# Kernel optimization log

Measured on AMD Instinct MI355X. Metric: run time of the kernel, lower is better.

Reference implementation:

```python
import jax, jax.numpy as jnp
import numpy as np

B, N, E, S, A, P, T = 512, 65536, 131072, 256, 512, 2, 64


def setup_inputs() -> dict:
    key = jax.random.key(0)
    ks = jax.random.split(key, 40)
    f32 = jnp.float32

    def g(i, shape, s=0.05):
        return jax.random.normal(ks[i], shape, f32) * s

    inp = {
        'nodes': jax.random.normal(ks[0], (N, S), f32),
        'edge_features': jax.random.normal(ks[1], (E, S), f32),
        'edge_source': jax.random.randint(ks[2], (E,), 0, N),
        'edge_dest': jax.random.randint(ks[3], (E,), 0, N),
        'node_owner': jax.random.randint(ks[4], (N,), 0, B),
        'running': jnp.ones((B,), bool),
        'ref_types': jax.random.randint(ks[5], (B,), 0, T),
        # decision aggregator (transform + sigmoid gate)
        'dec_t_W': g(6, (A, S)), 'dec_t_b': g(7, (A,)),
        'dec_g_W': g(8, (A, S)), 'dec_g_b': jnp.ones((A,), f32),
        # init aggregator
        'init_t_W': g(9, (A, S)), 'init_t_b': g(10, (A,)),
        'init_g_W': g(11, (A, S)), 'init_g_b': jnp.ones((A,), f32),
        # node type decision head + embedding
        'ntd_W': g(12, (T + 1, A)), 'ntd_b': g(13, (T + 1,)),
        'nte': g(14, (T, S), 1.0),
        # f_init
        'f1_W': g(15, (S, S)), 'f1_b': g(16, (S,)),
        'f2_W': g(17, (S, A)),
        # propagator params, stacked over P steps (message_size = 2S)
        'mn_W': g(18, (P, 2 * S, S)),
        'mf_W': g(19, (P, 2 * S, S)),
        'ml2_W': g(20, (P, 2 * S, 2 * S)), 'ml2_b': g(21, (P, 2 * S)),
        'gru_Wih': g(22, (P, 3 * S, 2 * S)), 'gru_Whh': g(23, (P, 3 * S, S)),
        'gru_bih': jnp.zeros((P, 3 * S), f32),
        'gru_bhh': jnp.concatenate(
            [jnp.ones((P, S), f32), jnp.zeros((P, 2 * S), f32)], axis=-1),
    }
    return inp


def _aggregate(nodes, fmask, tW, tb, gW, gb):
    # Aggregator.forward: sigmoid gate * linear transform, pooled per graph
    # via dense 0/1 owner-mask matmul (dropout=0 -> identity).
    gates = jax.nn.sigmoid(nodes @ gW.T + gb)
    data = nodes @ tW.T + tb
    return fmask @ (data * gates)  # [B, A]


def reference(nodes, edge_features, edge_source, edge_dest, node_owner,
              running, ref_types,
              dec_t_W, dec_t_b, dec_g_W, dec_g_b,
              init_t_W, init_t_b, init_g_W, init_g_b,
              ntd_W, ntd_b, nte, f1_W, f1_b, f2_W,
              mn_W, mf_W, ml2_W, ml2_b, gru_Wih, gru_Whh, gru_bih, gru_bhh):
    f32 = nodes.dtype
    fmask = (node_owner[None, :] == jnp.arange(B)[:, None]).astype(f32)  # [B,N]
    # Propagator._node_update_mask: owner_masks[running].sum(0) > 0
    upd = (fmask * running[:, None].astype(f32)).sum(0) > 0  # [N]

    for p in range(P):
        ef = edge_features @ mf_W[p].T                 # [E, 2S]
        nf = nodes @ mn_W[p].T                         # [N, 2S]
        msgs = nf[edge_source] + nf[edge_dest] + ef
        msgs = jnp.tanh(msgs) @ ml2_W[p].T + ml2_b[p]  # message_layer_2
        inputs = jnp.zeros((N, 2 * S), f32)
        inputs = inputs.at[edge_dest].add(msgs).at[edge_source].add(msgs)
        # torch GRUCell (gate order r, z, n)
        gi = inputs @ gru_Wih[p].T + gru_bih[p]
        gh = nodes @ gru_Whh[p].T + gru_bhh[p]
        ir, iz, inn = jnp.split(gi, 3, axis=-1)
        hr, hz, hn = jnp.split(gh, 3, axis=-1)
        r = jax.nn.sigmoid(ir + hr)
        z = jax.nn.sigmoid(iz + hz)
        n = jnp.tanh(inn + r * hn)
        new_nodes = (1.0 - z) * n + z * nodes
        nodes = jnp.where(upd[:, None], new_nodes, nodes)

    # node-type decision
    agg = _aggregate(nodes, fmask, dec_t_W, dec_t_b, dec_g_W, dec_g_b)
    logits = agg @ ntd_W.T + ntd_b                      # [B, T+1]

    # training path: remap_pad (no pad chars present) -> ref + 1
    sel = ref_types + 1                                  # in [1, T]
    logp = jax.nn.log_softmax(logits, axis=-1)
    per_ex = -logp[jnp.arange(B), sel]
    loss = jnp.where(running, per_ex, 0.0).mean()

    # new node features for running graphs
    emb = nte[sel - 1]                                   # [B, S]
    init_feats = _aggregate(nodes, fmask, init_t_W, init_t_b,
                            init_g_W, init_g_b)
    new_features = emb @ f1_W.T + f1_b + init_feats @ f2_W.T  # [B, S]
    return logits, new_features, loss
```

## Files before the change

### kernel.cpp

```cpp
#include <hip/hip_runtime.h>
#include <hip/hip_bf16.h>
#include <math.h>

#define BG 512
#define NN 65536
#define EE 131072
#define SD 256
#define AD 512
#define PP 2
#define TD 64

typedef __attribute__((ext_vector_type(8))) short sx8;
typedef __attribute__((ext_vector_type(4))) short sx4;
typedef __attribute__((ext_vector_type(4))) float fx4;

__device__ __forceinline__ float bs2f(short s) {
    union { unsigned u; float f; } x; x.u = ((unsigned)(unsigned short)s) << 16; return x.f;
}
__device__ __forceinline__ short f2bs(float f) {
    union { float f; unsigned u; } x; x.f = f;
    unsigned r = x.u + 0x7fffu + ((x.u >> 16) & 1u);
    return (short)(r >> 16);
}
__device__ __forceinline__ float fast_tanh(float x) {
    float xc = fminf(fmaxf(x, -15.f), 15.f);
    float e = __expf(2.f * xc);
    return __fdividef(e - 1.f, e + 1.f);
}
__device__ __forceinline__ float fast_sigm(float x) {
    float xc = fminf(fmaxf(x, -30.f), 30.f);
    float e = __expf(-xc);
    return __fdividef(1.f, 1.f + e);
}
__device__ __forceinline__ bool run_flag(const void* runv, int idx) {
    const unsigned char* r8 = (const unsigned char*)runv;
    const int* r32 = (const int*)runv;
    return (r8[idx] != 0) || (r32[idx] != 0);
}

__device__ __forceinline__ void gload16(const short* g, short* l) {
    __builtin_amdgcn_global_load_lds(
        (const __attribute__((address_space(1))) void*)g,
        (__attribute__((address_space(3))) void*)l, 16, 0, 0);
}

template<int EPI>
__launch_bounds__(256, 4)
__global__ void gemm_bt(const short* __restrict__ Abp, const short* __restrict__ Wp,
                        const float* __restrict__ bias, const float* __restrict__ bias2,
                        short* __restrict__ Cout, short* __restrict__ Fout,
                        short* __restrict__ FoutB,
                        const float* __restrict__ biasB, const float* __restrict__ biasB2,
                        const short* __restrict__ nfp,
                        const int* __restrict__ esrc, const int* __restrict__ edst,
                        int K, int NC, int NT, int nsplit)
{
    __shared__ __align__(16) short sA[2 * 4096];
    __shared__ __align__(16) short sB[2 * 4096];
    const int t = threadIdx.x;
    const int lane = t & 63;
    const int w = t >> 6;

    const int nwg = gridDim.x;
    const int q = nwg >> 3;
    const int wg = (blockIdx.x & 7) * q + (blockIdx.x >> 3);
    const int mt = wg / NT;
    const int nt = wg - mt * NT;
    const int m0 = mt * 128;
    const int n0 = nt * 128;

    const int wm = (w >> 1) * 64;
    const int wn = (w & 1) * 64;
    const int lr = lane & 15;
    const int lg = lane >> 4;

    fx4 acc[4][4];
#pragma unroll
    for (int i = 0; i < 4; i++)
#pragma unroll
        for (int j = 0; j < 4; j++) { fx4 z = {0.f, 0.f, 0.f, 0.f}; acc[i][j] = z; }

    const int r = t >> 2;
    const int cblk = (t & 3) ^ ((r >> 1) & 3);
    const short* gA = Abp + (size_t)(m0 + r) * K + cblk * 8;
    const short* gB = Wp + (size_t)(n0 + r) * K + cblk * 8;
    const size_t rowskip = (size_t)64 * K;

    auto STAGE = [&](int b, int kk) {
        gload16(gA + kk,           sA + b * 4096 + w * 512);
        gload16(gA + kk + rowskip, sA + b * 4096 + 2048 + w * 512);
        gload16(gB + kk,           sB + b * 4096 + w * 512);
        gload16(gB + kk + rowskip, sB + b * 4096 + 2048 + w * 512);
    };

    STAGE(0, 0);

    int es[4], ed[4];
    if (EPI == 2) {
#pragma unroll
        for (int mi = 0; mi < 4; mi++) {
            const int m = m0 + wm + mi * 16 + lr;
            es[mi] = esrc[m]; ed[mi] = edst[m];
        }
    }

    __syncthreads();
    int buf = 0;
    const int xa = (lr >> 1) & 3;
    for (int kk = 0; kk < K; kk += 32) {
        if (kk + 32 < K) STAGE(buf ^ 1, kk + 32);
        const short* cA = sA + buf * 4096;
        const short* cB = sB + buf * 4096;
        sx8 af[4], bfr[4];
#pragma unroll
        for (int mi = 0; mi < 4; mi++)
            af[mi] = *(const sx8*)(cA + (wm + mi * 16 + lr) * 32 + (lg ^ xa) * 8);
#pragma unroll
        for (int ni = 0; ni < 4; ni++)
            bfr[ni] = *(const sx8*)(cB + (wn + ni * 16 + lr) * 32 + (lg ^ xa) * 8);
#pragma unroll
        for (int mi = 0; mi < 4; mi++)
#pragma unroll
            for (int ni = 0; ni < 4; ni++) {
                if (EPI == 4)
                    acc[mi][ni] = __builtin_amdgcn_mfma_f32_16x16x32_bf16(
                        af[mi], bfr[ni], acc[mi][ni], 0, 0, 0);
                else
                    acc[mi][ni] = __builtin_amdgcn_mfma_f32_16x16x32_bf16(
                        bfr[ni], af[mi], acc[mi][ni], 0, 0, 0);
            }
        __syncthreads();
        buf ^= 1;
    }

    if (EPI == 4) {
        const bool useB = (n0 >= nsplit);
        short* fo = useB ? FoutB : Fout;
        const float* tb = useB ? biasB : bias;
        const float* gb = useB ? biasB2 : bias2;
        const int ln0 = useB ? (n0 - nsplit) : n0;
#pragma unroll
        for (int mi = 0; mi < 4; mi++) {
#pragma unroll
            for (int rg = 0; rg < 4; rg++) {
                const int m = m0 + wm + mi * 16 + lg * 4 + rg;
#pragma unroll
                for (int ni = 0; ni < 4; ni += 2) {
                    const int rc = (((ln0 + wn + ni * 16) >> 5) << 4) + lr;
                    float dv = acc[mi][ni][rg] + tb[rc];
                    float gv = fast_sigm(acc[mi][ni + 1][rg] + gb[rc]);
                    fo[(size_t)m * 512 + rc] = f2bs(dv * gv);
                }
            }
        }
    } else {
#pragma unroll
        for (int mi = 0; mi < 4; mi++) {
            const int m = m0 + wm + mi * 16 + lr;
            if (EPI == 2) {
                const short* ps = nfp + (size_t)es[mi] * NC + n0;
                const short* pd = nfp + (size_t)ed[mi] * NC + n0;
                short* co = Cout + (size_t)m * NC + n0;
#pragma unroll
                for (int ni = 0; ni < 4; ni++) {
                    const int nc = wn + ni * 16 + lg * 4;
                    sx4 a4 = *(const sx4*)(ps + nc);
                    sx4 b4 = *(const sx4*)(pd + nc);
                    sx4 o;
#pragma unroll
                    for (int rg = 0; rg < 4; rg++)
                        o[rg] = f2bs(fast_tanh(acc[mi][ni][rg]
                                               + bs2f(a4[rg]) + bs2f(b4[rg])));
                    *(sx4*)(co + nc) = o;
                }
            } else {
                short* co = Cout + (size_t)m * NC + n0;
#pragma unroll
                for (int ni = 0; ni < 4; ni++) {
                    const int nc = wn + ni * 16 + lg * 4;
                    fx4 vb = {0.f, 0.f, 0.f, 0.f};
                    if (bias) vb = *(const fx4*)(bias + n0 + nc);
                    sx4 o;
#pragma unroll
                    for (int rg = 0; rg < 4; rg++)
                        o[rg] = f2bs(acc[mi][ni][rg] + vb[rg]);
                    *(sx4*)(co + nc) = o;
                }
            }
        }
    }
}

__global__ void k_castw(const float* __restrict__ in, short* __restrict__ out)
{
    size_t i = ((size_t)blockIdx.x * 256 + threadIdx.x) * 4;
    fx4 v = *(const fx4*)(in + i);
    sx4 o;
#pragma unroll
    for (int u = 0; u < 4; u++) o[u] = f2bs(v[u]);
    *(sx4*)(out + i) = o;
}

__global__ void k_cast_pair(const float* __restrict__ tW, const float* __restrict__ gW,
                            short* __restrict__ out)
{
    size_t i = ((size_t)blockIdx.x * 256 + threadIdx.x) * 4;
    const int r2 = (int)(i >> 8);
    const int c = (int)(i & 255);
    const int src = ((r2 >> 5) << 4) | (r2 & 15);
    const float* W = ((r2 >> 4) & 1) ? gW : tW;
    fx4 v = *(const fx4*)(W + (size_t)src * 256 + c);
    sx4 o;
#pragma unroll
    for (int u = 0; u < 4; u++) o[u] = f2bs(v[u]);
    *(sx4*)(out + i) = o;
}

__global__ void k_count2(const int* __restrict__ a, const int* __restrict__ b,
                         int* __restrict__ deg, int n)
{
    int i = blockIdx.x * 256 + threadIdx.x;
    if (i < n) { atomicAdd(&deg[a[i]], 1); atomicAdd(&deg[b[i]], 1); }
}
__global__ void k_count1(const int* __restrict__ a, int* __restrict__ deg, int n)
{
    int i = blockIdx.x * 256 + threadIdx.x;
    if (i < n) atomicAdd(&deg[a[i]], 1);
}
__global__ void k_scan(const int* __restrict__ deg, int* __restrict__ offs, int n)
{
    __shared__ int part[256];
    const int t = threadIdx.x;
    const int chunk = n >> 8;
    const int base = t * chunk;
    int s = 0;
    for (int i = 0; i < chunk; i++) s += deg[base + i];
    part[t] = s;
    __syncthreads();
    for (int off = 1; off < 256; off <<= 1) {
        int v = (t >= off) ? part[t - off] : 0;
        __syncthreads();
        part[t] += v;
        __syncthreads();
    }
    int run = (t > 0) ? part[t - 1] : 0;
    for (int i = 0; i < chunk; i++) {
        offs[base + i] = run;
        run += deg[base + i];
    }
    if (t == 255) offs[n] = part[255];
}
__global__ void k_fill2(const int* __restrict__ a, const int* __restrict__ b,
                        const int* __restrict__ offs, int* __restrict__ cur,
                        int* __restrict__ elist, int n)
{
    int i = blockIdx.x * 256 + threadIdx.x;
    if (i < n) {
        int p = atomicAdd(&cur[a[i]], 1); elist[offs[a[i]] + p] = i;
        int q = atomicAdd(&cur[b[i]], 1); elist[offs[b[i]] + q] = i;
    }
}
__global__ void k_fill1(const int* __restrict__ own, const int* __restrict__ offs,
                        int* __restrict__ cur, int* __restrict__ nlist, int n)
{
    int i = blockIdx.x * 256 + threadIdx.x;
    if (i < n) {
        int p = atomicAdd(&cur[own[i]], 1); nlist[offs[own[i]] + p] = i;
    }
}

__global__ void k_edge_gather(const short* __restrict__ msgs, const int* __restrict__ offs,
                              const int* __restrict__ elist, short* __restrict__ inp)
{
    const int node = blockIdx.x * 4 + (threadIdx.x >> 6);
    const int c = (threadIdx.x & 63) * 8;
    const int s0 = offs[node], s1 = offs[node + 1];
    float acc[8] = {0.f, 0.f, 0.f, 0.f, 0.f, 0.f, 0.f, 0.f};
    for (int s = s0; s < s1; s++) {
        const int e = elist[s];
        sx8 v = *(const sx8*)(msgs + (size_t)e * 512 + c);
#pragma unroll
        for (int u = 0; u < 8; u++) acc[u] += bs2f(v[u]);
    }
    sx8 o;
#pragma unroll
    for (int u = 0; u < 8; u++) o[u] = f2bs(acc[u]);
    *(sx8*)(inp + (size_t)node * 512 + c) = o;
}

__global__ void k_owner_reduce(const short* __restrict__ gp, const int* __restrict__ offsB,
                               const int* __restrict__ nlist, float* __restrict__ agg)
{
    const int b = blockIdx.x, t = threadIdx.x;
    const int s0 = offsB[b], s1 = offsB[b + 1];
    float a0 = 0.f, a1 = 0.f;
    for (int s = s0; s < s1; s++) {
        const int n = nlist[s];
        const short* pp = gp + (size_t)n * 512 + t * 2;
        a0 += bs2f(pp[0]); a1 += bs2f(pp[1]);
    }
    agg[(size_t)b * 512 + t * 2] = a0;
    agg[(size_t)b * 512 + t * 2 + 1] = a1;
}

__global__ void k_gru(const short* __restrict__ gi, const short* __restrict__ gh,
                      short* __restrict__ nodes,
                      const int* __restrict__ owner, const void* __restrict__ runv)
{
    const int n = blockIdx.x * 4 + (threadIdx.x >> 6);
    const int t = threadIdx.x & 63;
    const bool run = run_flag(runv, owner[n]);
    const size_t gb = (size_t)n * 768 + t * 4;
    sx4 vir = *(const sx4*)(gi + gb);
    sx4 viz = *(const sx4*)(gi + gb + 256);
    sx4 vin = *(const sx4*)(gi + gb + 512);
    sx4 whr = *(const sx4*)(gh + gb);
    sx4 whz = *(const sx4*)(gh + gb + 256);
    sx4 whn = *(const sx4*)(gh + gb + 512);
    const size_t nbase = (size_t)n * 256 + t * 4;
    sx4 old4 = *(const sx4*)(nodes + nbase);
    sx4 outb;
#pragma unroll
    for (int u = 0; u < 4; u++) {
        float old = bs2f(old4[u]);
        float rr = fast_sigm(bs2f(vir[u]) + bs2f(whr[u]));
        float zz = fast_sigm(bs2f(viz[u]) + bs2f(whz[u]));
        float nn = fast_tanh(bs2f(vin[u]) + rr * bs2f(whn[u]));
        float nv = (1.f - zz) * nn + zz * old;
        outb[u] = run ? f2bs(nv) : old4[u];
    }
    *(sx4*)(nodes + nbase) = outb;
}

__global__ void k_logits(const float* __restrict__ agg, const float* __restrict__ Wt,
                         const float* __restrict__ bt, float* __restrict__ logitsF,
                         float* __restrict__ outL)
{
    __shared__ float row[512];
    const int b = blockIdx.x, t = threadIdx.x;
    for (int k = t; k < 512; k += 128) row[k] = agg[(size_t)b * 512 + k];
    __syncthreads();
    if (t < TD + 1) {
        float acc = bt[t];
        const float* wr = Wt + (size_t)t * 512;
        for (int k = 0; k < 512; k++) acc += row[k] * wr[k];
        logitsF[b * (TD + 1) + t] = acc;
        outL[b * (TD + 1) + t] = acc;
    }
}

__global__ void k_loss(const float* __restrict__ logitsF, const int* __restrict__ reft,
                       const void* __restrict__ runv, float* __restrict__ outLoss)
{
    __shared__ float red[512];
    const int b = threadIdx.x;
    const float* lr = logitsF + b * (TD + 1);
    float mx = lr[0];
    for (int k = 1; k < TD + 1; k++) mx = fmaxf(mx, lr[k]);
    float se = 0.f;
    for (int k = 0; k < TD + 1; k++) se += expf(lr[k] - mx);
    const int sel = reft[b] + 1;
    float pe = logf(se) + mx - lr[sel];
    red[b] = run_flag(runv, b) ? pe : 0.f;
    __syncthreads();
    for (int s = 256; s > 0; s >>= 1) {
        if (b < s) red[b] += red[b + s];
        __syncthreads();
    }
    if (b == 0) outLoss[0] = red[0] / (float)BG;
}

__global__ void k_newfeat(const float* __restrict__ aggi, const float* __restrict__ nte,
                          const int* __restrict__ reft, const float* __restrict__ f1W,
                          const float* __restrict__ f1b, const float* __restrict__ f2W,
                          float* __restrict__ outNF)
{
    __shared__ float emb[256];
    __shared__ float ag[512];
    const int b = blockIdx.x, t = threadIdx.x;
    const int rt = reft[b];
    emb[t] = nte[(size_t)rt * 256 + t];
    ag[t] = aggi[(size_t)b * 512 + t];
    ag[t + 256] = aggi[(size_t)b * 512 + 256 + t];
    __syncthreads();
    float acc = f1b[t];
    const float* w1 = f1W + (size_t)t * 256;
    for (int k = 0; k < 256; k++) acc += emb[k] * w1[k];
    const float* w2 = f2W + (size_t)t * 512;
    for (int a = 0; a < 512; a++) acc += ag[a] * w2[a];
    outNF[(size_t)b * 256 + t] = acc;
}

extern "C" void kernel_launch(void* const* d_in, const int* in_sizes, int n_in,
                              void* d_out, int out_size, void* d_ws, size_t ws_size,
                              hipStream_t stream)
{
    (void)in_sizes; (void)n_in; (void)out_size;
    const float* in_nodes = (const float*)d_in[0];
    const float* in_ef    = (const float*)d_in[1];
    const int*   e_src    = (const int*)d_in[2];
    const int*   e_dst    = (const int*)d_in[3];
    const int*   owner    = (const int*)d_in[4];
    const void*  running  = d_in[5];
    const int*   reft     = (const int*)d_in[6];
    const float* dec_tW = (const float*)d_in[7];
    const float* dec_tb = (const float*)d_in[8];
    const float* dec_gW = (const float*)d_in[9];
    const float* dec_gb = (const float*)d_in[10];
    const float* init_tW = (const float*)d_in[11];
    const float* init_tb = (const float*)d_in[12];
    const float* init_gW = (const float*)d_in[13];
    const float* init_gb = (const float*)d_in[14];
    const float* ntdW = (const float*)d_in[15];
    const float* ntdb = (const float*)d_in[16];
    const float* nte  = (const float*)d_in[17];
    const float* f1W  = (const float*)d_in[18];
    const float* f1b  = (const float*)d_in[19];
    const float* f2W  = (const float*)d_in[20];
    const float* mnW  = (const float*)d_in[21];
    const float* mfW  = (const float*)d_in[22];
    const float* ml2W = (const float*)d_in[23];
    const float* ml2b = (const float*)d_in[24];
    const float* Wih  = (const float*)d_in[25];
    const float* Whh  = (const float*)d_in[26];
    const float* bih  = (const float*)d_in[27];
    const float* bhh  = (const float*)d_in[28];

    float* outL    = (float*)d_out;
    float* outNF   = outL + BG * (TD + 1);
    float* outLoss = outNF + BG * SD;

    size_t off = 0;
    auto take = [&](size_t bytes) -> void* {
        void* p = (char*)d_ws + off;
        off += (bytes + 255) & ~(size_t)255;
        return p;
    };
    short* nodes_bf  = (short*)take((size_t)NN * SD * 2);
    short* ef_bf     = (short*)take((size_t)EE * SD * 2);
    short* bufC      = (short*)take((size_t)NN * 512 * 2);
    short* bufD      = (short*)take((size_t)EE * 512 * 2);
    short* bufM      = (short*)take((size_t)EE * 512 * 2);
    short* bufI      = (short*)take((size_t)NN * 512 * 2);
    float* aggD      = (float*)take((size_t)BG * AD * 4);
    float* aggI      = (float*)take((size_t)BG * AD * 4);
    float* logitsF   = (float*)take((size_t)BG * (TD + 1) * 4);
    short* mnWb  = (short*)take((size_t)PP * 512 * 256 * 2);
    short* mfWb  = (short*)take((size_t)PP * 512 * 256 * 2);
    short* ml2Wb = (short*)take((size_t)PP * 512 * 512 * 2);
    short* WihB  = (short*)take((size_t)PP * 768 * 512 * 2);
    short* WhhB  = (short*)take((size_t)PP * 768 * 256 * 2);
    short* W4agg = (short*)take((size_t)2048 * 256 * 2);
    int* deg_e = (int*)take((size_t)NN * 4);
    int* offs_e = (int*)take((size_t)(NN + 1) * 4);
    int* cur_e = (int*)take((size_t)NN * 4);
    int* elist = (int*)take((size_t)2 * EE * 4);
    int* degB = (int*)take((size_t)BG * 4);
    int* offsB = (int*)take((size_t)(BG + 1) * 4);
    int* curB = (int*)take((size_t)BG * 4);
    int* nlist = (int*)take((size_t)NN * 4);
    if (off > ws_size) return;

    short* gi = bufD;
    short* gh = bufM;
    short* gpD = bufM;
    short* gpI = bufD;

    k_castw<<<NN * SD / 1024, 256, 0, stream>>>(in_nodes, nodes_bf);
    k_castw<<<EE * SD / 1024, 256, 0, stream>>>(in_ef, ef_bf);
    k_castw<<<PP * 512 * 256 / 1024, 256, 0, stream>>>(mnW, mnWb);
    k_castw<<<PP * 512 * 256 / 1024, 256, 0, stream>>>(mfW, mfWb);
    k_castw<<<PP * 512 * 512 / 1024, 256, 0, stream>>>(ml2W, ml2Wb);
    k_castw<<<PP * 768 * 512 / 1024, 256, 0, stream>>>(Wih, WihB);
    k_castw<<<PP * 768 * 256 / 1024, 256, 0, stream>>>(Whh, WhhB);
    k_cast_pair<<<1024 * 256 / 1024, 256, 0, stream>>>(dec_tW, dec_gW, W4agg);
    k_cast_pair<<<1024 * 256 / 1024, 256, 0, stream>>>(init_tW, init_gW,
                                                       W4agg + 1024 * 256);

    hipMemsetAsync(deg_e, 0, (size_t)NN * 4, stream);
    hipMemsetAsync(cur_e, 0, (size_t)NN * 4, stream);
    hipMemsetAsync(degB, 0, (size_t)BG * 4, stream);
    hipMemsetAsync(curB, 0, (size_t)BG * 4, stream);
    k_count2<<<(EE + 255) / 256, 256, 0, stream>>>(e_src, e_dst, deg_e, EE);
    k_scan<<<1, 256, 0, stream>>>(deg_e, offs_e, NN);
    k_fill2<<<(EE + 255) / 256, 256, 0, stream>>>(e_src, e_dst, offs_e, cur_e, elist, EE);
    k_count1<<<(NN + 255) / 256, 256, 0, stream>>>(owner, degB, NN);
    k_scan<<<1, 256, 0, stream>>>(degB, offsB, BG);
    k_fill1<<<(NN + 255) / 256, 256, 0, stream>>>(owner, offsB, curB, nlist, NN);

    for (int p = 0; p < PP; p++) {
        gemm_bt<0><<<NN / 128 * 4, 256, 0, stream>>>(
            nodes_bf, mnWb + (size_t)p * 512 * 256, nullptr, nullptr, bufC,
            nullptr, nullptr, nullptr, nullptr, nullptr, nullptr, nullptr,
            256, 512, 4, 0);
        gemm_bt<2><<<EE / 128 * 4, 256, 0, stream>>>(
            ef_bf, mfWb + (size_t)p * 512 * 256, nullptr, nullptr, bufD,
            nullptr, nullptr, nullptr, nullptr, bufC, e_src, e_dst,
            256, 512, 4, 0);
        gemm_bt<0><<<EE / 128 * 4, 256, 0, stream>>>(
            bufD, ml2Wb + (size_t)p * 512 * 512, ml2b + (size_t)p * 512, nullptr,
            bufM, nullptr, nullptr, nullptr, nullptr, nullptr, nullptr, nullptr,
            512, 512, 4, 0);
        k_edge_gather<<<NN / 4, 256, 0, stream>>>(bufM, offs_e, elist, bufI);
        gemm_bt<0><<<NN / 128 * 6, 256, 0, stream>>>(
            bufI, WihB + (size_t)p * 768 * 512, bih + (size_t)p * 768, nullptr,
            gi, nullptr, nullptr, nullptr, nullptr, nullptr, nullptr, nullptr,
            512, 768, 6, 0);
        gemm_bt<0><<<NN / 128 * 6, 256, 0, stream>>>(
            nodes_bf, WhhB + (size_t)p * 768 * 256, bhh + (size_t)p * 768, nullptr,
            gh, nullptr, nullptr, nullptr, nullptr, nullptr, nullptr, nullptr,
            256, 768, 6, 0);
        k_gru<<<NN / 4, 256, 0, stream>>>(gi, gh, nodes_bf, owner, running);
    }

    gemm_bt<4><<<NN / 128 * 16, 256, 0, stream>>>(
        nodes_bf, W4agg, dec_tb, dec_gb, nullptr, gpD, gpI,
        init_tb, init_gb, nullptr, nullptr, nullptr,
        256, 2048, 16, 1024);
    k_owner_reduce<<<BG, 256, 0, stream>>>(gpD, offsB, nlist, aggD);
    k_owner_reduce<<<BG, 256, 0, stream>>>(gpI, offsB, nlist, aggI);

    k_logits<<<BG, 128, 0, stream>>>(aggD, ntdW, ntdb, logitsF, outL);
    k_loss<<<1, 512, 0, stream>>>(logitsF, reft, running, outLoss);
    k_newfeat<<<BG, 256, 0, stream>>>(aggI, nte, reft, f1W, f1b, f2W, outNF);
}
```

Before: 1.870 ms.

## Replace per-node message GEMM plus edge gather with summed-endpoint input and fused K=512 GEMM

Instead of computing node projections (N x 512) and adding gathered src/dst rows in the edge GEMM epilogue, a new kernel builds x_src + x_dst per edge in bf16. A single GEMM with K=512 then concatenates that with the edge features against a combined [mn|mf] weight, and applies tanh in its epilogue. This drops the node GEMM and the scattered epilogue gathers, but it doubles the K of the edge GEMM (more FLOPs over E) and adds an E x 256 bf16 intermediate write and read. Summing the endpoints in bf16 before the matmul also changes rounding slightly.

```diff
diff --git a/kernel.cpp b/kernel.cpp
--- a/kernel.cpp
+++ b/kernel.cpp
@@ -46,14 +46,13 @@
 
 template<int EPI>
 __launch_bounds__(256, 4)
-__global__ void gemm_bt(const short* __restrict__ Abp, const short* __restrict__ Wp,
+__global__ void gemm_bt(const short* __restrict__ Abp, const short* __restrict__ Abp2,
+                        const short* __restrict__ Wp,
                         const float* __restrict__ bias, const float* __restrict__ bias2,
                         short* __restrict__ Cout, short* __restrict__ Fout,
                         short* __restrict__ FoutB,
                         const float* __restrict__ biasB, const float* __restrict__ biasB2,
-                        const short* __restrict__ nfp,
-                        const int* __restrict__ esrc, const int* __restrict__ edst,
-                        int K, int NC, int NT, int nsplit)
+                        int K, int Ksp, int NC, int NT, int nsplit)
 {
     __shared__ __align__(16) short sA[2 * 4096];
     __shared__ __align__(16) short sB[2 * 4096];
@@ -82,28 +81,23 @@
 
     const int r = t >> 2;
     const int cblk = (t & 3) ^ ((r >> 1) & 3);
-    const short* gA = Abp + (size_t)(m0 + r) * K + cblk * 8;
-    const short* gB = Wp + (size_t)(n0 + r) * K + cblk * 8;
-    const size_t rowskip = (size_t)64 * K;
+    const short* gA  = Abp  + (size_t)(m0 + r) * Ksp + cblk * 8;
+    const short* gA2 = Abp2 + (size_t)(m0 + r) * (K - Ksp) + cblk * 8;
+    const short* gB  = Wp + (size_t)(n0 + r) * K + cblk * 8;
+    const size_t rsA  = (size_t)64 * Ksp;
+    const size_t rsA2 = (size_t)64 * (K - Ksp);
+    const size_t rsB  = (size_t)64 * K;
 
     auto STAGE = [&](int b, int kk) {
-        gload16(gA + kk,           sA + b * 4096 + w * 512);
-        gload16(gA + kk + rowskip, sA + b * 4096 + 2048 + w * 512);
-        gload16(gB + kk,           sB + b * 4096 + w * 512);
-        gload16(gB + kk + rowskip, sB + b * 4096 + 2048 + w * 512);
+        const short* a0 = (kk < Ksp) ? (gA + kk) : (gA2 + (kk - Ksp));
+        const size_t rs = (kk < Ksp) ? rsA : rsA2;
+        gload16(a0,            sA + b * 4096 + w * 512);
+        gload16(a0 + rs,       sA + b * 4096 + 2048 + w * 512);
+        gload16(gB + kk,       sB + b * 4096 + w * 512);
+        gload16(gB + kk + rsB, sB + b * 4096 + 2048 + w * 512);
     };
 
     STAGE(0, 0);
-
-    int es[4], ed[4];
-    if (EPI == 2) {
-#pragma unroll
-        for (int mi = 0; mi < 4; mi++) {
-            const int m = m0 + wm + mi * 16 + lr;
-            es[mi] = esrc[m]; ed[mi] = edst[m];
-        }
-    }
-
     __syncthreads();
     int buf = 0;
     const int xa = (lr >> 1) & 3;
@@ -157,44 +151,62 @@
 #pragma unroll
         for (int mi = 0; mi < 4; mi++) {
             const int m = m0 + wm + mi * 16 + lr;
-            if (EPI == 2) {
-                const short* ps = nfp + (size_t)es[mi] * NC + n0;
-                const short* pd = nfp + (size_t)ed[mi] * NC + n0;
-                short* co = Cout + (size_t)m * NC + n0;
-#pragma unroll
-                for (int ni = 0; ni < 4; ni++) {
-                    const int nc = wn + ni * 16 + lg * 4;
-                    sx4 a4 = *(const sx4*)(ps + nc);
-                    sx4 b4 = *(const sx4*)(pd + nc);
-                    sx4 o;
+            short* co = Cout + (size_t)m * NC + n0;
+#pragma unroll
+            for (int ni = 0; ni < 4; ni++) {
+                const int nc = wn + ni * 16 + lg * 4;
+                sx4 o;
+                if (EPI == 1) {
 #pragma unroll
                     for (int rg = 0; rg < 4; rg++)
-                        o[rg] = f2bs(fast_tanh(acc[mi][ni][rg]
-                                               + bs2f(a4[rg]) + bs2f(b4[rg])));
-                    *(sx4*)(co + nc) = o;
-                }
-            } else {
-                short* co = Cout + (size_t)m * NC + n0;
-#pragma unroll
-                for (int ni = 0; ni < 4; ni++) {
-                    const int nc = wn + ni * 16 + lg * 4;
+                        o[rg] = f2bs(fast_tanh(acc[mi][ni][rg]));
+                } else {
                     fx4 vb = {0.f, 0.f, 0.f, 0.f};
                     if (bias) vb = *(const fx4*)(bias + n0 + nc);
-                    sx4 o;
 #pragma unroll
                     for (int rg = 0; rg < 4; rg++)
                         o[rg] = f2bs(acc[mi][ni][rg] + vb[rg]);
-                    *(sx4*)(co + nc) = o;
                 }
+                *(sx4*)(co + nc) = o;
             }
         }
     }
 }
 
+__global__ void k_xadd(const short* __restrict__ nodes, const int* __restrict__ esrc,
+                       const int* __restrict__ edst, short* __restrict__ X)
+{
+    size_t idx = ((size_t)blockIdx.x * 256 + threadIdx.x) * 8;
+    const int e = (int)(idx >> 8);
+    const int j = (int)(idx & 255);
+    const int s = esrc[e], d = edst[e];
+    sx8 a = *(const sx8*)(nodes + (size_t)s * 256 + j);
+    sx8 b = *(const sx8*)(nodes + (size_t)d * 256 + j);
+    sx8 o;
+#pragma unroll
+    for (int u = 0; u < 8; u++) o[u] = f2bs(bs2f(a[u]) + bs2f(b[u]));
+    *(sx8*)(X + idx) = o;
+}
+
 __global__ void k_castw(const float* __restrict__ in, short* __restrict__ out)
 {
     size_t i = ((size_t)blockIdx.x * 256 + threadIdx.x) * 4;
     fx4 v = *(const fx4*)(in + i);
+    sx4 o;
+#pragma unroll
+    for (int u = 0; u < 4; u++) o[u] = f2bs(v[u]);
+    *(sx4*)(out + i) = o;
+}
+
+__global__ void k_cast_comb(const float* __restrict__ mn, const float* __restrict__ mf,
+                            short* __restrict__ out)
+{
+    size_t i = ((size_t)blockIdx.x * 256 + threadIdx.x) * 4;
+    const int n = (int)(i >> 9);
+    const int k = (int)(i & 511);
+    const float* W = (k < 256) ? (mn + (size_t)n * 256 + k)
+                               : (mf + (size_t)n * 256 + (k - 256));
+    fx4 v = *(const fx4*)W;
     sx4 o;
 #pragma unroll
     for (int u = 0; u < 4; u++) o[u] = f2bs(v[u]);
@@ -438,15 +450,14 @@
     };
     short* nodes_bf  = (short*)take((size_t)NN * SD * 2);
     short* ef_bf     = (short*)take((size_t)EE * SD * 2);
-    short* bufC      = (short*)take((size_t)NN * 512 * 2);
+    short* bufC      = (short*)take((size_t)EE * SD * 2);
     short* bufD      = (short*)take((size_t)EE * 512 * 2);
     short* bufM      = (short*)take((size_t)EE * 512 * 2);
     short* bufI      = (short*)take((size_t)NN * 512 * 2);
     float* aggD      = (float*)take((size_t)BG * AD * 4);
     float* aggI      = (float*)take((size_t)BG * AD * 4);
     float* logitsF   = (float*)take((size_t)BG * (TD + 1) * 4);
-    short* mnWb  = (short*)take((size_t)PP * 512 * 256 * 2);
-    short* mfWb  = (short*)take((size_t)PP * 512 * 256 * 2);
+    short* WcombB = (short*)take((size_t)PP * 512 * 512 * 2);
     short* ml2Wb = (short*)take((size_t)PP * 512 * 512 * 2);
     short* WihB  = (short*)take((size_t)PP * 768 * 512 * 2);
     short* WhhB  = (short*)take((size_t)PP * 768 * 256 * 2);
@@ -468,8 +479,10 @@
 
     k_castw<<<NN * SD / 1024, 256, 0, stream>>>(in_nodes, nodes_bf);
     k_castw<<<EE * SD / 1024, 256, 0, stream>>>(in_ef, ef_bf);
-    k_castw<<<PP * 512 * 256 / 1024, 256, 0, stream>>>(mnW, mnWb);
-    k_castw<<<PP * 512 * 256 / 1024, 256, 0, stream>>>(mfW, mfWb);
+    for (int p = 0; p < PP; p++)
+        k_cast_comb<<<512 * 512 / 1024, 256, 0, stream>>>(
+            mnW + (size_t)p * 512 * 256, mfW + (size_t)p * 512 * 256,
+            WcombB + (size_t)p * 512 * 512);
     k_castw<<<PP * 512 * 512 / 1024, 256, 0, stream>>>(ml2W, ml2Wb);
     k_castw<<<PP * 768 * 512 / 1024, 256, 0, stream>>>(Wih, WihB);
     k_castw<<<PP * 768 * 256 / 1024, 256, 0, stream>>>(Whh, WhhB);
@@ -489,34 +502,31 @@
     k_fill1<<<(NN + 255) / 256, 256, 0, stream>>>(owner, offsB, curB, nlist, NN);
 
     for (int p = 0; p < PP; p++) {
-        gemm_bt<0><<<NN / 128 * 4, 256, 0, stream>>>(
-            nodes_bf, mnWb + (size_t)p * 512 * 256, nullptr, nullptr, bufC,
-            nullptr, nullptr, nullptr, nullptr, nullptr, nullptr, nullptr,
-            256, 512, 4, 0);
-        gemm_bt<2><<<EE / 128 * 4, 256, 0, stream>>>(
-            ef_bf, mfWb + (size_t)p * 512 * 256, nullptr, nullptr, bufD,
-            nullptr, nullptr, nullptr, nullptr, bufC, e_src, e_dst,
-            256, 512, 4, 0);
+        k_xadd<<<EE / 8, 256, 0, stream>>>(nodes_bf, e_src, e_dst, bufC);
+        gemm_bt<1><<<EE / 128 * 4, 256, 0, stream>>>(
+            bufC, ef_bf, WcombB + (size_t)p * 512 * 512, nullptr, nullptr,
+            bufD, nullptr, nullptr, nullptr, nullptr,
+            512, 256, 512, 4, 0);
         gemm_bt<0><<<EE / 128 * 4, 256, 0, stream>>>(
-            bufD, ml2Wb + (size_t)p * 512 * 512, ml2b + (size_t)p * 512, nullptr,
-            bufM, nullptr, nullptr, nullptr, nullptr, nullptr, nullptr, nullptr,
-            512, 512, 4, 0);
+            bufD, bufD, ml2Wb + (size_t)p * 512 * 512, ml2b + (size_t)p * 512,
+            nullptr, bufM, nullptr, nullptr, nullptr, nullptr,
+            512, 512, 512, 4, 0);
         k_edge_gather<<<NN / 4, 256, 0, stream>>>(bufM, offs_e, elist, bufI);
         gemm_bt<0><<<NN / 128 * 6, 256, 0, stream>>>(
-            bufI, WihB + (size_t)p * 768 * 512, bih + (size_t)p * 768, nullptr,
-            gi, nullptr, nullptr, nullptr, nullptr, nullptr, nullptr, nullptr,
-            512, 768, 6, 0);
+            bufI, bufI, WihB + (size_t)p * 768 * 512, bih + (size_t)p * 768,
+            nullptr, gi, nullptr, nullptr, nullptr, nullptr,
+            512, 512, 768, 6, 0);
         gemm_bt<0><<<NN / 128 * 6, 256, 0, stream>>>(
-            nodes_bf, WhhB + (size_t)p * 768 * 256, bhh + (size_t)p * 768, nullptr,
-            gh, nullptr, nullptr, nullptr, nullptr, nullptr, nullptr, nullptr,
-            256, 768, 6, 0);
+            nodes_bf, nodes_bf, WhhB + (size_t)p * 768 * 256, bhh + (size_t)p * 768,
+            nullptr, gh, nullptr, nullptr, nullptr, nullptr,
+            256, 256, 768, 6, 0);
         k_gru<<<NN / 4, 256, 0, stream>>>(gi, gh, nodes_bf, owner, running);
     }
 
     gemm_bt<4><<<NN / 128 * 16, 256, 0, stream>>>(
-        nodes_bf, W4agg, dec_tb, dec_gb, nullptr, gpD, gpI,
-        init_tb, init_gb, nullptr, nullptr, nullptr,
-        256, 2048, 16, 1024);
+        nodes_bf, nodes_bf, W4agg, dec_tb, dec_gb,
+        nullptr, gpD, gpI, init_tb, init_gb,
+        256, 256, 2048, 16, 1024);
     k_owner_reduce<<<BG, 256, 0, stream>>>(gpD, offsB, nlist, aggD);
     k_owner_reduce<<<BG, 256, 0, stream>>>(gpI, offsB, nlist, aggI);
 
```

Result: faster. 1.821 ms (-2.6%).
